# Kernel tuning notes

Hardware: AMD Instinct MI355X
Metric: run time of the kernel (lower is better)

## Reference

```python
import jax, jax.numpy as jnp
import numpy as np

N_NODES = 50000
NEG_SLOPE = 0.2  # PyG GATConv default


def setup_inputs() -> dict:
    key = jax.random.key(0)
    ks = jax.random.split(key, 10)
    N, D_IN, HID, H, D_OUT, E = N_NODES, 256, 64, 4, 40, 800000
    inp = {
        "x": jax.random.normal(ks[0], (N, D_IN), jnp.float32),
        "edge_index": jax.random.randint(ks[1], (2, E), 0, N, jnp.int32),
        "W1": jax.random.normal(ks[2], (D_IN, H * HID), jnp.float32) * (1.0 / np.sqrt(D_IN)),
        "att_src1": jax.random.normal(ks[3], (H, HID), jnp.float32) * 0.1,
        "att_dst1": jax.random.normal(ks[4], (H, HID), jnp.float32) * 0.1,
        "b1": jnp.zeros((H * HID,), jnp.float32),
        "W2": jax.random.normal(ks[5], (H * HID, D_OUT), jnp.float32) * (1.0 / np.sqrt(H * HID)),
        "att_src2": jax.random.normal(ks[6], (1, D_OUT), jnp.float32) * 0.1,
        "att_dst2": jax.random.normal(ks[7], (1, D_OUT), jnp.float32) * 0.1,
        "b2": jnp.zeros((D_OUT,), jnp.float32),
    }
    return inp


def _gat_conv(x, src, dst, W, a_src, a_dst, b, n_nodes):
    """One GATConv layer (PyG semantics, self-loops already in src/dst)."""
    H, F = a_src.shape
    h = (x @ W).reshape(n_nodes, H, F)                      # [N,H,F]
    a_s = jnp.einsum('nhf,hf->nh', h, a_src)                # [N,H]
    a_d = jnp.einsum('nhf,hf->nh', h, a_dst)                # [N,H]
    e = jax.nn.leaky_relu(a_s[src] + a_d[dst], NEG_SLOPE)   # [E,H]
    # segment softmax over incoming edges of each destination node
    m = jax.ops.segment_max(e, dst, num_segments=n_nodes)   # [N,H]
    ex = jnp.exp(e - m[dst])                                # [E,H]
    den = jax.ops.segment_sum(ex, dst, num_segments=n_nodes)
    alpha = ex / den[dst]                                   # [E,H]
    out = jax.ops.segment_sum(h[src] * alpha[:, :, None], dst, num_segments=n_nodes)
    return out.reshape(n_nodes, H * F) + b


def reference(x, edge_index, W1, att_src1, att_dst1, b1, W2, att_src2, att_dst2, b2):
    N = x.shape[0]
    loop = jnp.arange(N, dtype=edge_index.dtype)
    src = jnp.concatenate([edge_index[0], loop])
    dst = jnp.concatenate([edge_index[1], loop])
    h = jax.nn.relu(_gat_conv(x, src, dst, W1, att_src1, att_dst1, b1, N))
    logits = _gat_conv(h, src, dst, W2, att_src2, att_dst2, b2, N)
    return jax.nn.log_softmax(logits, axis=1)
```

## Files before the change

kernel.cpp:

```cpp
#include <hip/hip_runtime.h>
#include <hip/hip_fp16.h>
#include <math.h>

#define NEG_SLOPE 0.2f

typedef short short8v __attribute__((ext_vector_type(8)));
typedef _Float16 half8v __attribute__((ext_vector_type(8)));
typedef float f32x4 __attribute__((ext_vector_type(4)));

__device__ __forceinline__ unsigned short f2bf(float f) {
    unsigned int u = __builtin_bit_cast(unsigned int, f);
    u += 0x7FFFu + ((u >> 16) & 1u);
    return (unsigned short)(u >> 16);
}

__device__ __forceinline__ void fma_h4(float4& acc, float w, uint2 v) {
    __half2 p0 = __builtin_bit_cast(__half2, v.x);
    __half2 p1 = __builtin_bit_cast(__half2, v.y);
    float2 f0 = __half22float2(p0), f1 = __half22float2(p1);
    acc.x += w * f0.x; acc.y += w * f0.y; acc.z += w * f1.x; acc.w += w * f1.y;
}

__global__ void k_deg(const int* __restrict__ ei, int E, int N, int* __restrict__ deg, int* __restrict__ rank) {
    int i = blockIdx.x * blockDim.x + threadIdx.x;
    int Et = E + N;
    if (i >= Et) return;
    int dst = (i < E) ? ei[E + i] : (i - E);
    rank[i] = atomicAdd(&deg[dst], 1);
}

__global__ void k_scan_block(const int* __restrict__ deg, int N, int* __restrict__ excl, int* __restrict__ bsums) {
    __shared__ int s[256];
    int b = blockIdx.x, t = threadIdx.x;
    int i = b * 256 + t;
    int v = (i < N) ? deg[i] : 0;
    s[t] = v;
    __syncthreads();
    for (int off = 1; off < 256; off <<= 1) {
        int add = (t >= off) ? s[t - off] : 0;
        __syncthreads();
        s[t] += add;
        __syncthreads();
    }
    int incl = s[t];
    if (i < N) excl[i] = incl - v;
    if (t == 255) bsums[b] = incl;
}

__global__ void k_scan_sums(int* __restrict__ bsums, int NB) {
    __shared__ int s[256];
    int t = threadIdx.x;
    int v = (t < NB) ? bsums[t] : 0;
    s[t] = v;
    __syncthreads();
    for (int off = 1; off < 256; off <<= 1) {
        int add = (t >= off) ? s[t - off] : 0;
        __syncthreads();
        s[t] += add;
        __syncthreads();
    }
    if (t < NB) bsums[t] = s[t] - v;
}

__global__ void k_scan_add(int* __restrict__ row_start, const int* __restrict__ bsums, int N, int Et) {
    int i = blockIdx.x * blockDim.x + threadIdx.x;
    if (i < N) row_start[i] += bsums[blockIdx.x];
    if (i == 0) row_start[N] = Et;
}

__global__ void k_scatter(const int* __restrict__ ei, const int* __restrict__ rank, int E, int N,
                          const int* __restrict__ row_start, int* __restrict__ csr_src) {
    int i = blockIdx.x * blockDim.x + threadIdx.x;
    int Et = E + N;
    if (i >= Et) return;
    int src, dst;
    if (i < E) { src = ei[i]; dst = ei[E + i]; }
    else       { src = i - E; dst = i - E; }
    csr_src[row_start[dst] + rank[i]] = src;
}

__global__ void k_cvt_w(const float* __restrict__ W1, const float* __restrict__ W2,
                        unsigned short* __restrict__ w1t, __half* __restrict__ w2t) {
    int b = blockIdx.x, k = threadIdx.x;
    if (b < 256) {
        w1t[b * 256 + k] = f2bf(W1[k * 256 + b]);
    } else {
        int c = b - 256;
        w2t[c * 256 + k] = __float2half((c < 40) ? W2[k * 40 + c] : 0.f);
    }
}

#define LDP 264
__global__ __launch_bounds__(256) void k_gemm1_mfma(const float* __restrict__ x,
                                                    const unsigned short* __restrict__ w1t,
                                                    const float* __restrict__ att_s,
                                                    const float* __restrict__ att_d,
                                                    __half* __restrict__ h1h,
                                                    float* __restrict__ as1, float* __restrict__ ad1, int N) {
    __shared__ unsigned short As[64 * LDP];
    __shared__ unsigned short Bs[64 * LDP];
    int tid = threadIdx.x;
    int row0 = blockIdx.x * 64;
#pragma unroll
    for (int it = 0; it < 16; it++) {
        int c = tid + it * 256;
        int r = c >> 6, q = c & 63;
        float4 v = make_float4(0, 0, 0, 0);
        if (row0 + r < N) v = ((const float4*)x)[(size_t)(row0 + r) * 64 + q];
        ushort4 o;
        o.x = f2bf(v.x); o.y = f2bf(v.y); o.z = f2bf(v.z); o.w = f2bf(v.w);
        *(ushort4*)&As[r * LDP + q * 4] = o;
    }
    int w = tid >> 6, l = tid & 63;
    int hi = l >> 4, lo = l & 15;
    short8v a[8];
    for (int head = 0; head < 4; head++) {
#pragma unroll
        for (int it = 0; it < 8; it++) {
            int c = tid + it * 256;
            int r = c >> 5, q = c & 31;
            uint4 vb = ((const uint4*)w1t)[(size_t)(head * 64 + r) * 32 + q];
            *(uint4*)&Bs[r * LDP + q * 8] = vb;
        }
        __syncthreads();
        if (head == 0) {
#pragma unroll
            for (int kk = 0; kk < 8; kk++)
                a[kk] = *(const short8v*)&As[(16 * w + lo) * LDP + kk * 32 + 8 * hi];
        }
        f32x4 acc[4] = {};
#pragma unroll
        for (int kk = 0; kk < 8; kk++) {
#pragma unroll
            for (int jb = 0; jb < 4; jb++) {
                short8v b = *(const short8v*)&Bs[(16 * jb + lo) * LDP + kk * 32 + 8 * hi];
                acc[jb] = __builtin_amdgcn_mfma_f32_16x16x32_bf16(a[kk], b, acc[jb], 0, 0, 0);
            }
        }
        float asr[4], adr[4];
#pragma unroll
        for (int jb = 0; jb < 4; jb++) {
            int c = head * 64 + lo + 16 * jb;
            asr[jb] = att_s[c];
            adr[jb] = att_d[c];
        }
#pragma unroll
        for (int j = 0; j < 4; j++) {
            int rr = 16 * w + 4 * hi + j;
            int r = row0 + rr;
            float s = 0.f, d = 0.f;
#pragma unroll
            for (int jb = 0; jb < 4; jb++) {
                float v = acc[jb][j];
                s += v * asr[jb];
                d += v * adr[jb];
                if (r < N) h1h[(size_t)r * 256 + head * 64 + lo + 16 * jb] = __float2half(v);
            }
            s += __shfl_xor(s, 1); s += __shfl_xor(s, 2); s += __shfl_xor(s, 4); s += __shfl_xor(s, 8);
            d += __shfl_xor(d, 1); d += __shfl_xor(d, 2); d += __shfl_xor(d, 4); d += __shfl_xor(d, 8);
            if (lo == 0 && r < N) {
                as1[r * 4 + head] = s;
                ad1[r * 4 + head] = d;
            }
        }
        if (head < 3) __syncthreads();
    }
}

__global__ __launch_bounds__(256) void k_agg1(const __half* __restrict__ h1h, const float* __restrict__ as1,
                                              const float* __restrict__ ad1, const int* __restrict__ row_start,
                                              const int* __restrict__ csr_src, const float* __restrict__ b1,
                                              __half* __restrict__ hbh, int N) {
    __shared__ int    s_src[4][64];
    __shared__ float4 s_w[4][64];
    int wv = threadIdx.x >> 6, l = threadIdx.x & 63;
    int n = blockIdx.x * 4 + wv;
    if (n >= N) return;
    int s0 = row_start[n], s1 = row_start[n + 1];
    int head = l >> 4;
    unsigned lb8 = (unsigned)l * 8u;
    const char* h1b = (const char*)h1h;
    float4 adv = ((const float4*)ad1)[n];
    float4 acc0 = make_float4(0, 0, 0, 0), acc1 = acc0, acc2 = acc0, acc3 = acc0;
    float den = 0.f;
    for (int c0 = s0; c0 < s1; c0 += 64) {
        int cl = min(64, s1 - c0);
        if (l < cl) {
            int si = csr_src[c0 + l];
            s_src[wv][l] = si;
            float4 a = ((const float4*)as1)[si];
            float4 e;
            e.x = a.x + adv.x; e.x = e.x > 0.f ? e.x : NEG_SLOPE * e.x; e.x = __expf(e.x);
            e.y = a.y + adv.y; e.y = e.y > 0.f ? e.y : NEG_SLOPE * e.y; e.y = __expf(e.y);
            e.z = a.z + adv.z; e.z = e.z > 0.f ? e.z : NEG_SLOPE * e.z; e.z = __expf(e.z);
            e.w = a.w + adv.w; e.w = e.w > 0.f ? e.w : NEG_SLOPE * e.w; e.w = __expf(e.w);
            s_w[wv][l] = e;
        }
        int p = 0;
        for (; p + 8 <= cl; p += 8) {
            int ss[8]; float ww[8]; uint2 vv[8];
#pragma unroll
            for (int i = 0; i < 8; i++) {
                ss[i] = s_src[wv][p + i];
                ww[i] = ((const float*)&s_w[wv][p + i])[head];
            }
#pragma unroll
            for (int i = 0; i < 8; i++)
                vv[i] = *(const uint2*)(h1b + (unsigned)ss[i] * 512u + lb8);
#pragma unroll
            for (int i = 0; i < 8; i++) {
                den += ww[i];
                if ((i & 3) == 0) fma_h4(acc0, ww[i], vv[i]);
                if ((i & 3) == 1) fma_h4(acc1, ww[i], vv[i]);
                if ((i & 3) == 2) fma_h4(acc2, ww[i], vv[i]);
                if ((i & 3) == 3) fma_h4(acc3, ww[i], vv[i]);
            }
        }
        for (; p + 4 <= cl; p += 4) {
            int sA = s_src[wv][p],     sB = s_src[wv][p + 1];
            int sC = s_src[wv][p + 2], sD = s_src[wv][p + 3];
            float wA = ((const float*)&s_w[wv][p    ])[head];
            float wB = ((const float*)&s_w[wv][p + 1])[head];
            float wC = ((const float*)&s_w[wv][p + 2])[head];
            float wD = ((const float*)&s_w[wv][p + 3])[head];
            uint2 vA = *(const uint2*)(h1b + (unsigned)sA * 512u + lb8);
            uint2 vB = *(const uint2*)(h1b + (unsigned)sB * 512u + lb8);
            uint2 vC = *(const uint2*)(h1b + (unsigned)sC * 512u + lb8);
            uint2 vD = *(const uint2*)(h1b + (unsigned)sD * 512u + lb8);
            den += (wA + wB) + (wC + wD);
            fma_h4(acc0, wA, vA); fma_h4(acc1, wB, vB);
            fma_h4(acc2, wC, vC); fma_h4(acc3, wD, vD);
        }
        for (; p < cl; p++) {
            int s = s_src[wv][p];
            float wg = ((const float*)&s_w[wv][p])[head];
            uint2 v = *(const uint2*)(h1b + (unsigned)s * 512u + lb8);
            den += wg;
            fma_h4(acc0, wg, v);
        }
    }
    float4 acc;
    acc.x = (acc0.x + acc1.x) + (acc2.x + acc3.x);
    acc.y = (acc0.y + acc1.y) + (acc2.y + acc3.y);
    acc.z = (acc0.z + acc1.z) + (acc2.z + acc3.z);
    acc.w = (acc0.w + acc1.w) + (acc2.w + acc3.w);
    float inv = 1.f / den;
    float4 b = ((const float4*)b1)[l];
    float r0 = acc.x * inv + b.x; r0 = r0 > 0.f ? r0 : 0.f;
    float r1 = acc.y * inv + b.y; r1 = r1 > 0.f ? r1 : 0.f;
    float r2 = acc.z * inv + b.z; r2 = r2 > 0.f ? r2 : 0.f;
    float r3 = acc.w * inv + b.w; r3 = r3 > 0.f ? r3 : 0.f;
    unsigned short u0 = __builtin_bit_cast(unsigned short, __float2half(r0));
    unsigned short u1 = __builtin_bit_cast(unsigned short, __float2half(r1));
    unsigned short u2 = __builtin_bit_cast(unsigned short, __float2half(r2));
    unsigned short u3 = __builtin_bit_cast(unsigned short, __float2half(r3));
    uint2 st;
    st.x = (unsigned)u0 | ((unsigned)u1 << 16);
    st.y = (unsigned)u2 | ((unsigned)u3 << 16);
    *(uint2*)((char*)hbh + (unsigned)n * 512u + lb8) = st;
}

__global__ __launch_bounds__(256) void k_gemm2_mfma(const _Float16* __restrict__ hbh,
                                                    const _Float16* __restrict__ w2t,
                                                    const float* __restrict__ att_s2,
                                                    const float* __restrict__ att_d2,
                                                    __half* __restrict__ h2h,
                                                    float* __restrict__ as2, float* __restrict__ ad2, int N) {
    int tid = threadIdx.x, w = tid >> 6, l = tid & 63;
    int hi = l >> 4, lo = l & 15;
    int row0 = blockIdx.x * 64;
    int arow = row0 + 16 * w + lo;
    const char* hb = (const char*)hbh;
    f32x4 acc[3] = {};
#pragma unroll
    for (int kk = 0; kk < 8; kk++) {
        half8v a = {};
        if (arow < N) a = *(const half8v*)(hb + (unsigned)arow * 512u + (unsigned)(kk * 64 + 16 * hi));
#pragma unroll
        for (int jb = 0; jb < 3; jb++) {
            half8v b = *(const half8v*)&w2t[(16 * jb + lo) * 256 + kk * 32 + 8 * hi];
            acc[jb] = __builtin_amdgcn_mfma_f32_16x16x32_f16(a, b, acc[jb], 0, 0, 0);
        }
    }
    float asr[3], adr[3];
#pragma unroll
    for (int jb = 0; jb < 3; jb++) {
        int c = 16 * jb + lo;
        asr[jb] = (c < 40) ? att_s2[c] : 0.f;
        adr[jb] = (c < 40) ? att_d2[c] : 0.f;
    }
#pragma unroll
    for (int j = 0; j < 4; j++) {
        int r = row0 + 16 * w + 4 * hi + j;
        float s = 0.f, d = 0.f;
#pragma unroll
        for (int jb = 0; jb < 3; jb++) {
            float v = acc[jb][j];
            s += v * asr[jb];
            d += v * adr[jb];
            int c = 16 * jb + lo;
            if (c < 40 && r < N) h2h[(size_t)r * 40 + c] = __float2half(v);
        }
        s += __shfl_xor(s, 1); s += __shfl_xor(s, 2); s += __shfl_xor(s, 4); s += __shfl_xor(s, 8);
        d += __shfl_xor(d, 1); d += __shfl_xor(d, 2); d += __shfl_xor(d, 4); d += __shfl_xor(d, 8);
        if (lo == 0 && r < N) { as2[r] = s; ad2[r] = d; }
    }
}

__global__ __launch_bounds__(256) void k_agg2(const __half* __restrict__ h2h, const float* __restrict__ as2,
                                              const float* __restrict__ ad2, const int* __restrict__ row_start,
                                              const int* __restrict__ csr_src, const float* __restrict__ b2,
                                              float* __restrict__ out, int N) {
    __shared__ int   s_src[4][64];
    __shared__ float s_w[4][64];
    int wv = threadIdx.x >> 6, l = threadIdx.x & 63;
    int n = blockIdx.x * 4 + wv;
    if (n >= N) return;
    int s0 = row_start[n], s1 = row_start[n + 1];
    int grp = l / 20, li = l - grp * 20;
    unsigned li4 = (unsigned)li * 4u;
    const char* h2b = (const char*)h2h;
    float ad = ad2[n];
    float2 accA = make_float2(0.f, 0.f), accB = accA;
    float denA = 0.f, denB = 0.f;
    bool act = grp < 3;
    for (int c0 = s0; c0 < s1; c0 += 64) {
        int cl = min(64, s1 - c0);
        if (l < cl) {
            int si = csr_src[c0 + l];
            s_src[wv][l] = si;
            float e = as2[si] + ad;
            e = e > 0.f ? e : NEG_SLOPE * e;
            s_w[wv][l] = __expf(e);
        }
        if (act) {
            int p = grp;
            for (; p + 3 < cl; p += 6) {
                int sA = s_src[wv][p], sB = s_src[wv][p + 3];
                float wA = s_w[wv][p], wB = s_w[wv][p + 3];
                unsigned vA = *(const unsigned*)(h2b + (unsigned)sA * 80u + li4);
                unsigned vB = *(const unsigned*)(h2b + (unsigned)sB * 80u + li4);
                denA += wA; denB += wB;
                float2 fA = __half22float2(__builtin_bit_cast(__half2, vA));
                float2 fB = __half22float2(__builtin_bit_cast(__half2, vB));
                accA.x += wA * fA.x; accA.y += wA * fA.y;
                accB.x += wB * fB.x; accB.y += wB * fB.y;
            }
            for (; p < cl; p += 3) {
                int si = s_src[wv][p];
                float w = s_w[wv][p];
                unsigned v = *(const unsigned*)(h2b + (unsigned)si * 80u + li4);
                denA += w;
                float2 f = __half22float2(__builtin_bit_cast(__half2, v));
                accA.x += w * f.x; accA.y += w * f.y;
            }
        }
    }
    float den = denA + denB;
    float2 acc = make_float2(accA.x + accB.x, accA.y + accB.y);
    float den_t = __shfl(den, li) + __shfl(den, 20 + li) + __shfl(den, 40 + li);
    float ax = acc.x + __shfl(acc.x, l + 20) + __shfl(acc.x, l + 40);
    float ay = acc.y + __shfl(acc.y, l + 20) + __shfl(acc.y, l + 40);
    float inv = 1.f / den_t;
    float lg0 = -1e30f, lg1 = -1e30f;
    if (l < 20) {
        lg0 = ax * inv + b2[2 * l];
        lg1 = ay * inv + b2[2 * l + 1];
    }
    float mx = fmaxf(lg0, lg1);
    for (int off = 32; off; off >>= 1) mx = fmaxf(mx, __shfl_xor(mx, off));
    float s = (l < 20) ? (__expf(lg0 - mx) + __expf(lg1 - mx)) : 0.f;
    for (int off = 32; off; off >>= 1) s += __shfl_xor(s, off);
    float ls = logf(s);
    if (l < 20) {
        out[(size_t)n * 40 + 2 * l]     = lg0 - mx - ls;
        out[(size_t)n * 40 + 2 * l + 1] = lg1 - mx - ls;
    }
}

extern "C" void kernel_launch(void* const* d_in, const int* in_sizes, int n_in,
                              void* d_out, int out_size, void* d_ws, size_t ws_size,
                              hipStream_t stream) {
    const float* x      = (const float*)d_in[0];
    const int*   ei     = (const int*)d_in[1];
    const float* W1     = (const float*)d_in[2];
    const float* att_s1 = (const float*)d_in[3];
    const float* att_d1 = (const float*)d_in[4];
    const float* b1     = (const float*)d_in[5];
    const float* W2     = (const float*)d_in[6];
    const float* att_s2 = (const float*)d_in[7];
    const float* att_d2 = (const float*)d_in[8];
    const float* b2     = (const float*)d_in[9];

    int N = in_sizes[0] / 256;
    int E = in_sizes[1] / 2;
    int Et = E + N;

    char* ws = (char*)d_ws;
    size_t off = 0;
    auto alloc = [&](size_t bytes) -> void* {
        void* p = ws + off;
        off += (bytes + 255) / 256 * 256;
        return p;
    };
    __half* h1h = (__half*)alloc((size_t)N * 256 * 2);
    __half* hbh = (__half*)alloc((size_t)N * 256 * 2);
    __half* h2h = (__half*)alloc((size_t)N * 40 * 2);
    unsigned short* w1t = (unsigned short*)alloc((size_t)256 * 256 * 2);
    __half* w2t = (__half*)alloc((size_t)48 * 256 * 2);
    float* as1 = (float*)alloc((size_t)N * 4 * 4);
    float* ad1 = (float*)alloc((size_t)N * 4 * 4);
    float* as2 = (float*)alloc((size_t)N * 4);
    float* ad2 = (float*)alloc((size_t)N * 4);
    int* deg       = (int*)alloc((size_t)N * 4);
    int* rank      = (int*)alloc((size_t)Et * 4);
    int* row_start = (int*)alloc((size_t)(N + 1) * 4);
    int* csr_src   = (int*)alloc((size_t)Et * 4);
    int NB = (N + 255) / 256;
    int* bsums = (int*)alloc((size_t)NB * 4);

    hipMemsetAsync(deg, 0, (size_t)N * 4, stream);

    k_deg<<<(Et + 255) / 256, 256, 0, stream>>>(ei, E, N, deg, rank);
    k_scan_block<<<NB, 256, 0, stream>>>(deg, N, row_start, bsums);
    k_scan_sums<<<1, 256, 0, stream>>>(bsums, NB);
    k_scan_add<<<NB, 256, 0, stream>>>(row_start, bsums, N, Et);
    k_scatter<<<(Et + 255) / 256, 256, 0, stream>>>(ei, rank, E, N, row_start, csr_src);

    k_cvt_w<<<304, 256, 0, stream>>>(W1, W2, w1t, w2t);

    k_gemm1_mfma<<<(N + 63) / 64, 256, 0, stream>>>(x, w1t, att_s1, att_d1, h1h, as1, ad1, N);
    k_agg1<<<(N + 3) / 4, 256, 0, stream>>>(h1h, as1, ad1, row_start, csr_src, b1, hbh, N);
    k_gemm2_mfma<<<(N + 63) / 64, 256, 0, stream>>>((const _Float16*)hbh, (const _Float16*)w2t,
                                                    att_s2, att_d2, h2h, as2, ad2, N);
    k_agg2<<<(N + 3) / 4, 256, 0, stream>>>(h2h, as2, ad2, row_start, csr_src, b2, (float*)d_out, N);
}
```

Before: 211.8 us.

## Fuse degree count with weight conversion, merge scan kernels, stage GEMM2 tiles in LDS

Merges the weight conversion kernel into the degree-counting kernel by adding extra blocks. It also removes the separate block-sums scan kernel: each add block now reduces the preceding block sums itself with wave shuffles. Together these cut two launches from the preprocessing chain. GEMM2 now stages its 64-row activation tile and the transposed W2 into padded shared memory before the MFMA loop, replacing strided global loads, at the cost of more LDS per block.

```diff
diff --git a/kernel.cpp b/kernel.cpp
--- a/kernel.cpp
+++ b/kernel.cpp
@@ -21,12 +21,27 @@
     acc.x += w * f0.x; acc.y += w * f0.y; acc.z += w * f1.x; acc.w += w * f1.y;
 }
 
-__global__ void k_deg(const int* __restrict__ ei, int E, int N, int* __restrict__ deg, int* __restrict__ rank) {
-    int i = blockIdx.x * blockDim.x + threadIdx.x;
-    int Et = E + N;
-    if (i >= Et) return;
-    int dst = (i < E) ? ei[E + i] : (i - E);
-    rank[i] = atomicAdd(&deg[dst], 1);
+__global__ void k_deg_cvt(const int* __restrict__ ei, int E, int N, int degB,
+                          int* __restrict__ deg, int* __restrict__ rank,
+                          const float* __restrict__ W1, const float* __restrict__ W2,
+                          unsigned short* __restrict__ w1t, __half* __restrict__ w2t) {
+    int b = blockIdx.x;
+    if (b < degB) {
+        int i = b * 256 + threadIdx.x;
+        int Et = E + N;
+        if (i >= Et) return;
+        int dst = (i < E) ? ei[E + i] : (i - E);
+        rank[i] = atomicAdd(&deg[dst], 1);
+    } else {
+        int bb = b - degB;
+        int k = threadIdx.x;
+        if (bb < 256) {
+            w1t[bb * 256 + k] = f2bf(W1[k * 256 + bb]);
+        } else {
+            int c = bb - 256;
+            w2t[c * 256 + k] = __float2half((c < 40) ? W2[k * 40 + c] : 0.f);
+        }
+    }
 }
 
 __global__ void k_scan_block(const int* __restrict__ deg, int N, int* __restrict__ excl, int* __restrict__ bsums) {
@@ -47,24 +62,18 @@
     if (t == 255) bsums[b] = incl;
 }
 
-__global__ void k_scan_sums(int* __restrict__ bsums, int NB) {
-    __shared__ int s[256];
-    int t = threadIdx.x;
-    int v = (t < NB) ? bsums[t] : 0;
-    s[t] = v;
+__global__ void k_scan_add(int* __restrict__ row_start, const int* __restrict__ bsums,
+                           int N, int Et, int NB) {
+    __shared__ int ws[4];
+    int b = blockIdx.x, t = threadIdx.x;
+    int wv = t >> 6, l = t & 63;
+    int v = (t < b && t < NB) ? bsums[t] : 0;
+    for (int off = 32; off; off >>= 1) v += __shfl_xor(v, off);
+    if (l == 0) ws[wv] = v;
     __syncthreads();
-    for (int off = 1; off < 256; off <<= 1) {
-        int add = (t >= off) ? s[t - off] : 0;
-        __syncthreads();
-        s[t] += add;
-        __syncthreads();
-    }
-    if (t < NB) bsums[t] = s[t] - v;
-}
-
-__global__ void k_scan_add(int* __restrict__ row_start, const int* __restrict__ bsums, int N, int Et) {
-    int i = blockIdx.x * blockDim.x + threadIdx.x;
-    if (i < N) row_start[i] += bsums[blockIdx.x];
+    int total = ws[0] + ws[1] + ws[2] + ws[3];
+    int i = b * 256 + t;
+    if (i < N) row_start[i] += total;
     if (i == 0) row_start[N] = Et;
 }
 
@@ -77,17 +86,6 @@
     if (i < E) { src = ei[i]; dst = ei[E + i]; }
     else       { src = i - E; dst = i - E; }
     csr_src[row_start[dst] + rank[i]] = src;
-}
-
-__global__ void k_cvt_w(const float* __restrict__ W1, const float* __restrict__ W2,
-                        unsigned short* __restrict__ w1t, __half* __restrict__ w2t) {
-    int b = blockIdx.x, k = threadIdx.x;
-    if (b < 256) {
-        w1t[b * 256 + k] = f2bf(W1[k * 256 + b]);
-    } else {
-        int c = b - 256;
-        w2t[c * 256 + k] = __float2half((c < 40) ? W2[k * 40 + c] : 0.f);
-    }
 }
 
 #define LDP 264
@@ -266,19 +264,35 @@
                                                     const float* __restrict__ att_d2,
                                                     __half* __restrict__ h2h,
                                                     float* __restrict__ as2, float* __restrict__ ad2, int N) {
-    int tid = threadIdx.x, w = tid >> 6, l = tid & 63;
+    __shared__ _Float16 Hs[64 * LDP];
+    __shared__ _Float16 Ws[48 * LDP];
+    int tid = threadIdx.x;
+    int row0 = blockIdx.x * 64;
+#pragma unroll
+    for (int it = 0; it < 8; it++) {
+        int c = tid + it * 256;
+        int r = c >> 5, q = c & 31;
+        uint4 v = make_uint4(0, 0, 0, 0);
+        if (row0 + r < N) v = ((const uint4*)hbh)[(size_t)(row0 + r) * 32 + q];
+        *(uint4*)&Hs[r * LDP + q * 8] = v;
+    }
+#pragma unroll
+    for (int it = 0; it < 6; it++) {
+        int c = tid + it * 256;
+        int r = c >> 5, q = c & 31;
+        uint4 v = ((const uint4*)w2t)[c];
+        *(uint4*)&Ws[r * LDP + q * 8] = v;
+    }
+    __syncthreads();
+    int w = tid >> 6, l = tid & 63;
     int hi = l >> 4, lo = l & 15;
-    int row0 = blockIdx.x * 64;
-    int arow = row0 + 16 * w + lo;
-    const char* hb = (const char*)hbh;
     f32x4 acc[3] = {};
 #pragma unroll
     for (int kk = 0; kk < 8; kk++) {
-        half8v a = {};
-        if (arow < N) a = *(const half8v*)(hb + (unsigned)arow * 512u + (unsigned)(kk * 64 + 16 * hi));
+        half8v a = *(const half8v*)&Hs[(16 * w + lo) * LDP + kk * 32 + 8 * hi];
 #pragma unroll
         for (int jb = 0; jb < 3; jb++) {
-            half8v b = *(const half8v*)&w2t[(16 * jb + lo) * 256 + kk * 32 + 8 * hi];
+            half8v b = *(const half8v*)&Ws[(16 * jb + lo) * LDP + kk * 32 + 8 * hi];
             acc[jb] = __builtin_amdgcn_mfma_f32_16x16x32_f16(a, b, acc[jb], 0, 0, 0);
         }
     }
@@ -421,13 +435,11 @@
 
     hipMemsetAsync(deg, 0, (size_t)N * 4, stream);
 
-    k_deg<<<(Et + 255) / 256, 256, 0, stream>>>(ei, E, N, deg, rank);
+    int degB = (Et + 255) / 256;
+    k_deg_cvt<<<degB + 304, 256, 0, stream>>>(ei, E, N, degB, deg, rank, W1, W2, w1t, w2t);
     k_scan_block<<<NB, 256, 0, stream>>>(deg, N, row_start, bsums);
-    k_scan_sums<<<1, 256, 0, stream>>>(bsums, NB);
-    k_scan_add<<<NB, 256, 0, stream>>>(row_start, bsums, N, Et);
+    k_scan_add<<<NB, 256, 0, stream>>>(row_start, bsums, N, Et, NB);
     k_scatter<<<(Et + 255) / 256, 256, 0, stream>>>(ei, rank, E, N, row_start, csr_src);
-
-    k_cvt_w<<<304, 256, 0, stream>>>(W1, W2, w1t, w2t);
 
     k_gemm1_mfma<<<(N + 63) / 64, 256, 0, stream>>>(x, w1t, att_s1, att_d1, h1h, as1, ad1, N);
     k_agg1<<<(N + 3) / 4, 256, 0, stream>>>(h1h, as1, ad1, row_start, csr_src, b1, hbh, N);
```

New measurement: 202.6 us. 1.05x faster.
